# Optimization experiments

Hardware: AMD Instinct MI355X
Metric: run time of the kernel (lower is better)

The kernel has to match this reference:

```python
import jax, jax.numpy as jnp
import numpy as np

NLAT, NLON = 361, 720
LMAX = NLAT
MMAX = min(LMAX, NLON // 2 + 1)


def _clenshaw_curtiss_weights(n):
    # Waldvogel fast Clenshaw-Curtis nodes/weights on [-1, 1]
    tcc = np.cos(np.linspace(np.pi, 0, n))
    n1 = n - 1
    N = np.arange(1, n1, 2)
    num_odd = len(N)
    m = n1 - num_odd
    v = np.concatenate([2 / N / (N - 2), 1 / N[-1:], np.zeros(m)])
    v = 0 - v[:-1] - v[-1:0:-1]
    g0 = -1 * np.ones(n1)
    g0[num_odd] += n1
    g0[m] += n1
    g = g0 / (n1 ** 2 - 1 + n1 % 2)
    wcc = np.fft.ifft(v + g).real
    wcc = np.concatenate((wcc, wcc[:1]))
    return tcc, wcc


def _legpoly(mmax, lmax, x):
    # associated Legendre values (-1)^m c^l_m P^l_m(x), ortho norm, CS phase on
    nmax = max(mmax, lmax)
    vdm = np.zeros((nmax, nmax, len(x)), dtype=np.float64)
    vdm[0, 0, :] = 1.0 / np.sqrt(4 * np.pi)
    for n in range(1, nmax):
        vdm[n - 1, n, :] = np.sqrt(2 * n + 1) * x * vdm[n - 1, n - 1, :]
        vdm[n, n, :] = np.sqrt((2 * n + 1) * (1 + x) * (1 - x) / 2 / n) * vdm[n - 1, n - 1, :]
    for n in range(2, nmax):
        for m in range(0, n - 1):
            a = np.sqrt((2 * n - 1) / (n - m) * (2 * n + 1) / (n + m))
            b = np.sqrt((n + m - 1) / (n - m) * (2 * n + 1) / (2 * n - 3) * (n - m - 1) / (n + m))
            vdm[m, n, :] = x * a * vdm[m, n - 1, :] - b * vdm[m, n - 2, :]
    vdm = vdm[:mmax, :lmax]
    for m in range(1, mmax, 2):
        vdm[m] *= -1
    return vdm


def _build_weights():
    cost, w = _clenshaw_curtiss_weights(NLAT)
    tq = np.flip(np.arccos(cost))
    pct = _legpoly(MMAX, LMAX, np.cos(tq))  # (mmax, lmax, nlat)
    return jnp.asarray(pct * w[None, None, :], dtype=jnp.float32)


def setup_inputs() -> dict:
    key = jax.random.key(0)
    x = jax.random.normal(key, (1, 32, NLAT, NLON), dtype=jnp.float32)
    weights = _build_weights()
    return {"x": x, "weights": weights}


def reference(x, weights):
    # rfft over longitude, 'forward' norm, scaled by 2*pi
    xf = 2.0 * jnp.pi * jnp.fft.rfft(x, axis=-1, norm='forward')  # [..., nlat, nlon//2+1]
    xf = xf[..., :MMAX]  # [..., k=nlat, m=mmax]
    # per-order Legendre contraction over latitude k, real and imag separately
    out_re = jnp.einsum('...km,mlk->...lm', jnp.real(xf), weights)
    out_im = jnp.einsum('...km,mlk->...lm', jnp.imag(xf), weights)
    # complex spectral coefficients [..., lmax, mmax] returned as real/imag pair
    return jnp.stack([out_re, out_im], axis=-1)
```

## Files before the change

### kernel.cpp

```cpp
#include <hip/hip_runtime.h>

#define NLAT 361
#define NLON 720
#define NF   361
#define NCH  32
#define NCK  (NCH * NLAT)
#define KP   384
#define KD   768
#define MD   384
#define AROW 392
#define BROW 72

typedef _Float16 h16;
typedef _Float16 f16x2 __attribute__((ext_vector_type(2)));
typedef _Float16 f16x4 __attribute__((ext_vector_type(4)));
typedef _Float16 f16x8 __attribute__((ext_vector_type(8)));
typedef float    f32x4 __attribute__((ext_vector_type(4)));

#define PLANE ((size_t)NF * NCH * KP)

__global__ __launch_bounds__(256) void k_build_T(
    h16* __restrict__ Tre, h16* __restrict__ Tim) {
    int idx = blockIdx.x * 256 + threadIdx.x;
    if (idx >= MD * KD) return;
    int f = idx / KD, n = idx - f * KD;
    float re = 0.f, im = 0.f;
    if (f < NF && n < NLON) {
        int j = (f * n) % NLON;
        float ang = -6.283185307179586f * ((float)j / (float)NLON);
        float s, c;
        sincosf(ang, &s, &c);
        const float scale = 6.283185307179586f / (float)NLON;
        re = c * scale; im = s * scale;
    }
    Tre[idx] = (h16)re;
    Tim[idx] = (h16)im;
}

__global__ __launch_bounds__(256) void k_stage1m(
    const float* __restrict__ x, const h16* __restrict__ Tre,
    const h16* __restrict__ Tim, h16* __restrict__ xfh) {
    __shared__ h16 As[2][64][BROW];
    __shared__ h16 Bs[64][BROW];
    const int t    = threadIdx.x;
    const int f0   = blockIdx.x * 64;
    const int n0   = blockIdx.y * 64;
    const int lane = t & 63, wv = t >> 6;
    const int wm   = wv & 1, wn = wv >> 1;
    const int col  = lane & 15, kq = lane >> 4;

    f32x4 acc[2][2][2];
    #pragma unroll
    for (int p = 0; p < 2; ++p)
        #pragma unroll
        for (int a = 0; a < 2; ++a)
            #pragma unroll
            for (int b = 0; b < 2; ++b) acc[p][a][b] = (f32x4)0.0f;

    for (int ks = 0; ks < 12; ++ks) {
        __syncthreads();
        #pragma unroll
        for (int i = 0; i < 4; ++i) {
            int task = t + i * 256;
            int pl   = task >> 9;
            int rem  = task & 511;
            int r    = rem >> 3, ch = rem & 7;
            const h16* Tp = pl ? Tim : Tre;
            f16x8 v = *(const f16x8*)&Tp[(size_t)(f0 + r) * KD + ks * 64 + ch * 8];
            *(f16x8*)&As[pl][r][ch * 8] = v;
        }
        #pragma unroll
        for (int p = 0; p < 4; ++p) {
            int r = p * 16 + (t >> 4), c4 = t & 15;
            int rowg = n0 + r;
            int n = ks * 64 + c4 * 4;
            float4 v = make_float4(0.f, 0.f, 0.f, 0.f);
            if (rowg < NCK && n < NLON)
                v = *(const float4*)&x[(size_t)rowg * NLON + n];
            f16x4 h = { (h16)v.x, (h16)v.y, (h16)v.z, (h16)v.w };
            *(f16x4*)&Bs[r][c4 * 4] = h;
        }
        __syncthreads();
        #pragma unroll
        for (int kk = 0; kk < 2; ++kk) {
            f16x8 bfr[2], afr[2][2];
            #pragma unroll
            for (int nt = 0; nt < 2; ++nt)
                bfr[nt] = *(const f16x8*)&Bs[wn * 32 + nt * 16 + col][kk * 32 + kq * 8];
            #pragma unroll
            for (int pl = 0; pl < 2; ++pl)
                #pragma unroll
                for (int mt = 0; mt < 2; ++mt)
                    afr[pl][mt] = *(const f16x8*)&As[pl][wm * 32 + mt * 16 + col][kk * 32 + kq * 8];
            #pragma unroll
            for (int pl = 0; pl < 2; ++pl)
                #pragma unroll
                for (int mt = 0; mt < 2; ++mt)
                    #pragma unroll
                    for (int nt = 0; nt < 2; ++nt)
                        acc[pl][mt][nt] = __builtin_amdgcn_mfma_f32_16x16x32_f16(
                            afr[pl][mt], bfr[nt], acc[pl][mt][nt], 0, 0, 0);
        }
    }

    #pragma unroll
    for (int nt = 0; nt < 2; ++nt) {
        int rowg = n0 + wn * 32 + nt * 16 + col;
        if (rowg >= NCK) continue;
        int c    = rowg / NLAT;
        int klat = rowg - c * NLAT;
        size_t cbase = (size_t)c * KP + klat;
        #pragma unroll
        for (int pl = 0; pl < 2; ++pl)
            #pragma unroll
            for (int mt = 0; mt < 2; ++mt)
                #pragma unroll
                for (int r = 0; r < 4; ++r) {
                    int f = f0 + wm * 32 + mt * 16 + kq * 4 + r;
                    if (f < NF)
                        xfh[(size_t)pl * PLANE + (size_t)f * NCH * KP + cbase] =
                            (h16)acc[pl][mt][nt][r];
                }
    }
}

__global__ __launch_bounds__(512, 4) void k_stage2(
    const h16* __restrict__ xfh, const float* __restrict__ W,
    f16x2* __restrict__ outws) {
    __shared__ h16 Ah[2 * NCH * AROW];
    const int b   = blockIdx.x;
    const int xcd = b & 7, ii = b >> 3;
    const int bid = (xcd == 0) ? ii : (90 + (xcd - 1) * 89 + ii);
    int m, g;
    if (bid < 336)      { m = bid / 3;                g = bid - 3 * m; }
    else if (bid < 592) { int r = bid - 336; m = 112 + (r >> 1); g = r & 1; }
    else                { m = 240 + (bid - 592);      g = 0; }

    const int t     = threadIdx.x;
    const int lane  = t & 63;
    const int wv    = t >> 6;
    const int lt    = (m >> 4) + g * 8 + wv;
    const bool ok   = (lt <= 22);
    const int col   = lane & 15;
    const int krow  = lane >> 4;
    const int krow8 = krow * 8;

    const float* Wm = W + (size_t)m * NLAT * NLAT;
    const int l     = lt * 16 + col;
    const int lsafe = (l < NLAT) ? l : (NLAT - 1);
    const float* wrow = Wm + (size_t)lsafe * NLAT + krow8;

    #pragma unroll
    for (int i = 0; i < 6; ++i) {
        int task = t + i * 512;
        int ri   = task / 1536;
        int rem  = task - ri * 1536;
        int c    = rem / 48, k8 = rem - c * 48;
        f16x8 v;
        if (k8 < 46) {
            v = *(const f16x8*)&xfh[(size_t)ri * PLANE + ((size_t)(m * NCH + c)) * KP + k8 * 8];
        } else {
            #pragma unroll
            for (int e = 0; e < 8; ++e) v[e] = (h16)0.f;
        }
        if (k8 == 45) {
            #pragma unroll
            for (int e = 1; e < 8; ++e) v[e] = (h16)0.f;
        }
        *(f16x8*)&Ah[(ri * NCH + c) * AROW + k8 * 8] = v;
    }

    f16x8 wh[12];
    float wa[16], wb[16];
    if (ok) {
        #pragma unroll
        for (int e = 0; e < 16; ++e) wa[e] = wrow[(e >> 3) * 32 + (e & 7)];
        #pragma unroll
        for (int e = 0; e < 16; ++e) wb[e] = wrow[(2 + (e >> 3)) * 32 + (e & 7)];
    } else {
        #pragma unroll
        for (int e = 0; e < 16; ++e) { wa[e] = 0.f; wb[e] = 0.f; }
    }
    #pragma unroll
    for (int cc = 0; cc < 6; ++cc) {
        float* cur = (cc & 1) ? wb : wa;
        #pragma unroll
        for (int h = 0; h < 2; ++h)
            #pragma unroll
            for (int e = 0; e < 8; ++e)
                wh[cc * 2 + h][e] = (h16)cur[h * 8 + e];
        if (cc < 4 && ok) {
            #pragma unroll
            for (int e = 0; e < 16; ++e)
                cur[e] = wrow[((cc * 2 + 4) + (e >> 3)) * 32 + (e & 7)];
        }
    }

    f32x4 acc[2][2];
    #pragma unroll
    for (int ct = 0; ct < 2; ++ct)
        #pragma unroll
        for (int pl = 0; pl < 2; ++pl)
            acc[ct][pl] = (f32x4)0.0f;

    __syncthreads();

    #pragma unroll
    for (int ks = 0; ks < 12; ++ks) {
        f16x8 af[2][2];
        #pragma unroll
        for (int pl = 0; pl < 2; ++pl)
            #pragma unroll
            for (int ct = 0; ct < 2; ++ct)
                af[pl][ct] = *(const f16x8*)&Ah[(pl * NCH + ct * 16 + col) * AROW + ks * 32 + krow8];

        #pragma unroll
        for (int ct = 0; ct < 2; ++ct)
            #pragma unroll
            for (int pl = 0; pl < 2; ++pl)
                acc[ct][pl] = __builtin_amdgcn_mfma_f32_16x16x32_f16(
                    af[pl][ct], wh[ks], acc[ct][pl], 0, 0, 0);
    }

    if (ok && l < NLAT) {
        #pragma unroll
        for (int ct = 0; ct < 2; ++ct) {
            #pragma unroll
            for (int r = 0; r < 4; ++r) {
                int c = ct * 16 + krow * 4 + r;
                f16x2 p;
                p[0] = (h16)acc[ct][0][r];
                p[1] = (h16)acc[ct][1][r];
                outws[((size_t)m * NCH + c) * NLAT + l] = p;
            }
        }
    }
}

__global__ __launch_bounds__(256) void k_transpose(
    const f16x2* __restrict__ src, float2* __restrict__ dst) {
    __shared__ f16x2 tile[32][33];
    const int tx = threadIdx.x & 31, ty = threadIdx.x >> 5;
    const int cl0 = blockIdx.x * 32, m0 = blockIdx.y * 32;
    #pragma unroll
    for (int i = 0; i < 4; ++i) {
        int mm = m0 + ty + i * 8;
        if (mm < NLAT) tile[ty + i * 8][tx] = src[(size_t)mm * NCK + cl0 + tx];
    }
    __syncthreads();
    #pragma unroll
    for (int i = 0; i < 4; ++i) {
        int mm = m0 + tx;
        int cl = cl0 + ty + i * 8;
        if (mm < NLAT) {
            int l = cl - (cl / NLAT) * NLAT;
            float2 v;
            if (l < mm) {
                v = make_float2(0.f, 0.f);
            } else {
                f16x2 p = tile[tx][ty + i * 8];
                v = make_float2((float)p[0], (float)p[1]);
            }
            dst[(size_t)cl * NLAT + mm] = v;
        }
    }
}

extern "C" void kernel_launch(void* const* d_in, const int* in_sizes, int n_in,
                              void* d_out, int out_size, void* d_ws, size_t ws_size,
                              hipStream_t stream) {
    const float* x = (const float*)d_in[0];
    const float* W = (const float*)d_in[1];
    float2* out2 = (float2*)d_out;

    char* ws = (char*)d_ws;
    h16*    Tre   = (h16*)(ws + 8192);
    h16*    Tim   = (h16*)(ws + 8192 + 589824);
    h16*    xfh   = (h16*)(ws + 1187840);
    f16x2*  outws = (f16x2*)(ws + 1187840 + 2 * PLANE * sizeof(h16));

    k_build_T<<<(MD * KD + 255) / 256, 256, 0, stream>>>(Tre, Tim);
    k_stage1m<<<dim3(6, 181), 256, 0, stream>>>(x, Tre, Tim, xfh);
    k_stage2<<<713, 512, 0, stream>>>(xfh, W, outws);
    k_transpose<<<dim3(361, 12), 256, 0, stream>>>(outws, out2);
}
```

Measured before the change: 92.78 us.

## Fold real DFT symmetry into even/odd inputs to halve DFT GEMM depth

Builds a new preprocessing kernel that forms x[n]+x[N-n] and x[n]-x[N-n] in fp16, then runs the DFT GEMM over 384 instead of 768 reduction points, using cosine and sine tables of half the length. Each plane now multiplies its own input (even with cosine, odd with sine), which halves the MFMA work and the table traffic in stage 1. In exchange it adds a separate conversion pass that writes about 17MB of fp16 intermediates and adds one more launch. Rounding the sums and differences to fp16 before the GEMM may slightly change accuracy.

```diff
diff --git a/kernel.cpp b/kernel.cpp
--- a/kernel.cpp
+++ b/kernel.cpp
@@ -6,7 +6,7 @@
 #define NCH  32
 #define NCK  (NCH * NLAT)
 #define KP   384
-#define KD   768
+#define KF   384
 #define MD   384
 #define AROW 392
 #define BROW 72
@@ -19,29 +19,51 @@
 
 #define PLANE ((size_t)NF * NCH * KP)
 
-__global__ __launch_bounds__(256) void k_build_T(
-    h16* __restrict__ Tre, h16* __restrict__ Tim) {
+__global__ __launch_bounds__(256) void k_build_T2(
+    h16* __restrict__ Tc, h16* __restrict__ Ts_) {
     int idx = blockIdx.x * 256 + threadIdx.x;
-    if (idx >= MD * KD) return;
-    int f = idx / KD, n = idx - f * KD;
-    float re = 0.f, im = 0.f;
-    if (f < NF && n < NLON) {
+    if (idx >= MD * KF) return;
+    int f = idx / KF, n = idx - f * KF;
+    float cv = 0.f, sv = 0.f;
+    if (f < NF && n <= 360) {
         int j = (f * n) % NLON;
         float ang = -6.283185307179586f * ((float)j / (float)NLON);
         float s, c;
         sincosf(ang, &s, &c);
         const float scale = 6.283185307179586f / (float)NLON;
-        re = c * scale; im = s * scale;
-    }
-    Tre[idx] = (h16)re;
-    Tim[idx] = (h16)im;
+        cv = c * scale;
+        sv = (n >= 1 && n <= 359) ? s * scale : 0.f;
+    }
+    Tc[idx]  = (h16)cv;
+    Ts_[idx] = (h16)sv;
+}
+
+__global__ __launch_bounds__(256) void k_convx(
+    const float* __restrict__ x, h16* __restrict__ xe, h16* __restrict__ xo) {
+    int tid = blockIdx.x * 256 + threadIdx.x;
+    if (tid >= NCK * 48) return;
+    int row = tid / 48, n8 = tid - row * 48;
+    const float* xr = x + (size_t)row * NLON;
+    f16x8 ve, vo;
+    #pragma unroll
+    for (int e = 0; e < 8; ++e) {
+        int n = n8 * 8 + e;
+        float a = 0.f, b = 0.f;
+        if (n == 0 || n == 360) { a = xr[n]; b = 0.f; }
+        else if (n < 360)       { a = xr[n] + xr[NLON - n]; b = xr[n] - xr[NLON - n]; }
+        ve[e] = (h16)a;
+        vo[e] = (h16)b;
+    }
+    *(f16x8*)&xe[(size_t)row * KF + n8 * 8] = ve;
+    *(f16x8*)&xo[(size_t)row * KF + n8 * 8] = vo;
 }
 
 __global__ __launch_bounds__(256) void k_stage1m(
-    const float* __restrict__ x, const h16* __restrict__ Tre,
-    const h16* __restrict__ Tim, h16* __restrict__ xfh) {
+    const h16* __restrict__ xe, const h16* __restrict__ xo,
+    const h16* __restrict__ Tc, const h16* __restrict__ Ts_,
+    h16* __restrict__ xfh) {
     __shared__ h16 As[2][64][BROW];
-    __shared__ h16 Bs[64][BROW];
+    __shared__ h16 Bs[2][64][BROW];
     const int t    = threadIdx.x;
     const int f0   = blockIdx.x * 64;
     const int n0   = blockIdx.y * 64;
@@ -57,7 +79,7 @@
             #pragma unroll
             for (int b = 0; b < 2; ++b) acc[p][a][b] = (f32x4)0.0f;
 
-    for (int ks = 0; ks < 12; ++ks) {
+    for (int ks = 0; ks < 6; ++ks) {
         __syncthreads();
         #pragma unroll
         for (int i = 0; i < 4; ++i) {
@@ -65,28 +87,36 @@
             int pl   = task >> 9;
             int rem  = task & 511;
             int r    = rem >> 3, ch = rem & 7;
-            const h16* Tp = pl ? Tim : Tre;
-            f16x8 v = *(const f16x8*)&Tp[(size_t)(f0 + r) * KD + ks * 64 + ch * 8];
+            const h16* Tp = pl ? Ts_ : Tc;
+            f16x8 v = *(const f16x8*)&Tp[(size_t)(f0 + r) * KF + ks * 64 + ch * 8];
             *(f16x8*)&As[pl][r][ch * 8] = v;
         }
         #pragma unroll
-        for (int p = 0; p < 4; ++p) {
-            int r = p * 16 + (t >> 4), c4 = t & 15;
+        for (int i = 0; i < 4; ++i) {
+            int task = t + i * 256;
+            int pl   = task >> 9;
+            int rem  = task & 511;
+            int r    = rem >> 3, ch = rem & 7;
             int rowg = n0 + r;
-            int n = ks * 64 + c4 * 4;
-            float4 v = make_float4(0.f, 0.f, 0.f, 0.f);
-            if (rowg < NCK && n < NLON)
-                v = *(const float4*)&x[(size_t)rowg * NLON + n];
-            f16x4 h = { (h16)v.x, (h16)v.y, (h16)v.z, (h16)v.w };
-            *(f16x4*)&Bs[r][c4 * 4] = h;
+            const h16* xp = pl ? xo : xe;
+            f16x8 v;
+            if (rowg < NCK) {
+                v = *(const f16x8*)&xp[(size_t)rowg * KF + ks * 64 + ch * 8];
+            } else {
+                #pragma unroll
+                for (int e = 0; e < 8; ++e) v[e] = (h16)0.f;
+            }
+            *(f16x8*)&Bs[pl][r][ch * 8] = v;
         }
         __syncthreads();
         #pragma unroll
         for (int kk = 0; kk < 2; ++kk) {
-            f16x8 bfr[2], afr[2][2];
-            #pragma unroll
-            for (int nt = 0; nt < 2; ++nt)
-                bfr[nt] = *(const f16x8*)&Bs[wn * 32 + nt * 16 + col][kk * 32 + kq * 8];
+            f16x8 bfr[2][2], afr[2][2];
+            #pragma unroll
+            for (int pl = 0; pl < 2; ++pl)
+                #pragma unroll
+                for (int nt = 0; nt < 2; ++nt)
+                    bfr[pl][nt] = *(const f16x8*)&Bs[pl][wn * 32 + nt * 16 + col][kk * 32 + kq * 8];
             #pragma unroll
             for (int pl = 0; pl < 2; ++pl)
                 #pragma unroll
@@ -99,7 +129,7 @@
                     #pragma unroll
                     for (int nt = 0; nt < 2; ++nt)
                         acc[pl][mt][nt] = __builtin_amdgcn_mfma_f32_16x16x32_f16(
-                            afr[pl][mt], bfr[nt], acc[pl][mt][nt], 0, 0, 0);
+                            afr[pl][mt], bfr[pl][nt], acc[pl][mt][nt], 0, 0, 0);
         }
     }
 
@@ -274,13 +304,16 @@
     float2* out2 = (float2*)d_out;
 
     char* ws = (char*)d_ws;
-    h16*    Tre   = (h16*)(ws + 8192);
-    h16*    Tim   = (h16*)(ws + 8192 + 589824);
-    h16*    xfh   = (h16*)(ws + 1187840);
-    f16x2*  outws = (f16x2*)(ws + 1187840 + 2 * PLANE * sizeof(h16));
-
-    k_build_T<<<(MD * KD + 255) / 256, 256, 0, stream>>>(Tre, Tim);
-    k_stage1m<<<dim3(6, 181), 256, 0, stream>>>(x, Tre, Tim, xfh);
+    h16*    Tc    = (h16*)(ws + 8192);
+    h16*    Ts_   = (h16*)(ws + 8192 + 294912);
+    h16*    xe16  = (h16*)(ws + 1187840);
+    h16*    xo16  = (h16*)(ws + 1187840 + 8871936);
+    h16*    xfh   = (h16*)(ws + 1187840 + 2 * 8871936);
+    f16x2*  outws = (f16x2*)(ws + 1187840 + 2 * 8871936 + 2 * PLANE * sizeof(h16));
+
+    k_build_T2<<<(MD * KF + 255) / 256, 256, 0, stream>>>(Tc, Ts_);
+    k_convx<<<(NCK * 48 + 255) / 256, 256, 0, stream>>>(x, xe16, xo16);
+    k_stage1m<<<dim3(6, 181), 256, 0, stream>>>(xe16, xo16, Tc, Ts_, xfh);
     k_stage2<<<713, 512, 0, stream>>>(xfh, W, outws);
     k_transpose<<<dim3(361, 12), 256, 0, stream>>>(outws, out2);
 }
```

Result: slower. 106.7 us (+15.0%).
